# Kernel tuning notes

Hardware: AMD Instinct MI355X
Metric: run time of the kernel (lower is better)

Reference implementation:

```python
import jax, jax.numpy as jnp
import numpy as np

B, T, N, D = 4, 12, 512, 128
L = 4            # max_lag + 1 lag encoders
H = D // 2       # lag-encoder hidden dim
THRESHOLD = 0.1


def setup_inputs() -> dict:
    key = jax.random.key(0)
    ks = jax.random.split(key, 10)
    s = 0.02
    return {
        "x":   jax.random.normal(ks[0], (B, T, N, D), dtype=jnp.float32),
        # lag encoders: Linear(D->H), ReLU, Linear(H->D), stacked over L lags
        "W1":  s * jax.random.normal(ks[1], (L, D, H), dtype=jnp.float32),
        "b1":  jnp.zeros((L, H), dtype=jnp.float32),
        "W2":  s * jax.random.normal(ks[2], (L, H, D), dtype=jnp.float32),
        "b2":  jnp.zeros((L, D), dtype=jnp.float32),
        # causal scorer: Linear(2D->D), ReLU, (Dropout=id in eval), Linear(D->1), Sigmoid
        "Ws1": s * jax.random.normal(ks[3], (2 * D, D), dtype=jnp.float32),
        "bs1": jnp.zeros((D,), dtype=jnp.float32),
        "Ws2": s * jax.random.normal(ks[4], (D, 1), dtype=jnp.float32),
        "bs2": jnp.zeros((1,), dtype=jnp.float32),
    }


def reference(x, W1, b1, W2, b2, Ws1, bs1, Ws2, bs2):
    Tdim = x.shape[1]
    # lagged slices x[:, T-1-lag] for lag in 0..L-1 (all lags active since T > max_lag)
    lags = jnp.stack([x[:, max(0, Tdim - 1 - l)] for l in range(L)], axis=1)  # (B,L,N,D)
    h = jax.nn.relu(jnp.einsum('blnd,ldh->blnh', lags, W1) + b1[None, :, None, :])
    enc = jnp.einsum('blnh,lhd->blnd', h, W2) + b2[None, :, None, :]          # (B,L,N,D)
    agg = enc.mean(axis=1)                                                    # (B,N,D)

    # pairwise causal scorer. cat([src, tgt]) @ Ws1 == src @ Ws1[:D] + tgt @ Ws1[D:],
    # avoiding the explicit (B,N,N,2D) concat.
    src_proj = jnp.einsum('bnd,dk->bnk', agg, Ws1[:D])   # (B,N,D)
    tgt_proj = jnp.einsum('bnd,dk->bnk', agg, Ws1[D:])   # (B,N,D)
    pre = src_proj[:, :, None, :] + tgt_proj[:, None, :, :] + bs1  # (B,N,N,D)
    score = jax.nn.sigmoid(jnp.einsum('bijd,d->bij', jax.nn.relu(pre), Ws2[:, 0]) + bs2[0])

    # threshold sparsification + remove self loops
    adj = jnp.where(score > THRESHOLD, score, 0.0)
    adj = adj * (1.0 - jnp.eye(N, dtype=adj.dtype))

    # multi-hop propagation and global max normalization per batch element
    a2 = jnp.matmul(adj, adj)
    a3 = jnp.matmul(a2, adj)
    enhanced = adj + 0.5 * a2 + 0.25 * a3
    mx = jnp.max(enhanced, axis=(-1, -2), keepdims=True)
    return enhanced / (mx + 1e-8)
```

## Files before the change

### kernel.cpp

```cpp
#include <hip/hip_runtime.h>
#include <math.h>

#define Bn 4
#define Tn 12
#define Nn 512
#define Dn 128
#define Ln 4
#define Hn 64

typedef __attribute__((ext_vector_type(8))) short short8;
typedef __attribute__((ext_vector_type(4))) float f32x4;
typedef _Float16 h2 __attribute__((ext_vector_type(2)));

__device__ __forceinline__ unsigned short f2bf(float f) {
    unsigned int u = __float_as_uint(f);
    unsigned int r = (u + 0x7FFF + ((u >> 16) & 1)) >> 16;
    return (unsigned short)r;
}
__device__ __forceinline__ float bf2f(unsigned short s) {
    return __uint_as_float(((unsigned int)s) << 16);
}
__device__ __forceinline__ float fdot2(h2 a, h2 b, float c) {
#if defined(__has_builtin)
#if __has_builtin(__builtin_amdgcn_fdot2)
    return __builtin_amdgcn_fdot2(a, b, c, false);
#else
    return c + (float)a.x*(float)b.x + (float)a.y*(float)b.y;
#endif
#else
    return c + (float)a.x*(float)b.x + (float)a.y*(float)b.y;
#endif
}

__global__ __launch_bounds__(256) void k_prep(
    const float* __restrict__ W1, const float* __restrict__ W2, const float* __restrict__ Ws1,
    unsigned short* __restrict__ w1p, unsigned short* __restrict__ w2p,
    unsigned short* __restrict__ wsp)
{
    int g = blockIdx.x*256 + threadIdx.x;
    unsigned short tmp[8];
    if (g < 4096) {
        int lag = g >> 10, r = g & 1023;
        int n = r >> 4, k8 = r & 15;
        #pragma unroll
        for (int j = 0; j < 8; ++j) tmp[j] = f2bf(W1[(size_t)(lag*128 + k8*8 + j)*64 + n]);
        *(short8*)(w1p + (size_t)lag*8192 + n*128 + k8*8) = *(const short8*)tmp;
    } else if (g < 8192) {
        int r = g - 4096;
        int n = r >> 5, k8 = r & 31;
        #pragma unroll
        for (int j = 0; j < 8; ++j) tmp[j] = f2bf(W2[(size_t)(k8*8 + j)*128 + n]);
        *(short8*)(w2p + (size_t)n*256 + k8*8) = *(const short8*)tmp;
    } else {
        int r = g - 8192;
        int tgt = r >> 11, r2 = r & 2047;
        int n = r2 >> 4, k8 = r2 & 15;
        #pragma unroll
        for (int j = 0; j < 8; ++j) tmp[j] = f2bf(Ws1[(size_t)(tgt*128 + k8*8 + j)*128 + n]);
        *(short8*)(wsp + (size_t)tgt*16384 + n*128 + k8*8) = *(const short8*)tmp;
    }
}

__global__ __launch_bounds__(512) void k_enc(
    const float* __restrict__ x,  const float* __restrict__ b1,
    const float* __restrict__ b2, const float* __restrict__ bs1,
    const unsigned short* __restrict__ w1p, const unsigned short* __restrict__ w2p,
    const unsigned short* __restrict__ wsp,
    unsigned short* __restrict__ spb, unsigned short* __restrict__ tpb,
    unsigned int* __restrict__ maxslot)
{
    __shared__ __align__(16) unsigned short xAll[4][16*136];
    __shared__ __align__(16) unsigned short hA[16*264];
    __shared__ __align__(16) unsigned short aggA[16*136];
    int tid  = threadIdx.x;
    int bid  = blockIdx.x;
    int wv   = __builtin_amdgcn_readfirstlane(tid >> 6);
    int lane = tid & 63;
    if (bid == 0 && tid < Bn) maxslot[tid] = 0u;

    int r0 = bid * 16;
    int bb = r0 >> 9, n0 = r0 & 511;
    int m = lane & 15, q = lane >> 4;
    int colL = lane & 15, rq = lane >> 4;

    for (int v = tid; v < 2048; v += 512) {
        int lag = v >> 9, r = v & 511;
        int row = r >> 5, c4 = r & 31;
        const float4* xs = (const float4*)(x + ((size_t)(bb*Tn + (Tn-1-lag))*Nn + n0)*Dn);
        float4 f = xs[row*32 + c4];
        ushort4 o = { f2bf(f.x), f2bf(f.y), f2bf(f.z), f2bf(f.w) };
        *(ushort4*)&xAll[lag][row*136 + c4*4] = o;
    }
    __syncthreads();

    {
        int lag = wv >> 1, hf = wv & 1;
        f32x4 acc[2] = {{0.f,0.f,0.f,0.f},{0.f,0.f,0.f,0.f}};
        #pragma unroll
        for (int ks = 0; ks < 4; ++ks) {
            short8 af = *(const short8*)&xAll[lag][m*136 + ks*32 + q*8];
            #pragma unroll
            for (int nt = 0; nt < 2; ++nt) {
                short8 bg = *(const short8*)(w1p + (size_t)lag*8192 + (hf*32 + nt*16 + m)*128 + ks*32 + q*8);
                acc[nt] = __builtin_amdgcn_mfma_f32_16x16x32_bf16(af, bg, acc[nt], 0, 0, 0);
            }
        }
        #pragma unroll
        for (int nt = 0; nt < 2; ++nt) {
            int ncol = hf*32 + nt*16 + colL;
            float bv = b1[lag*Hn + ncol];
            #pragma unroll
            for (int reg = 0; reg < 4; ++reg)
                hA[(rq*4+reg)*264 + lag*64 + ncol] = f2bf(fmaxf(acc[nt][reg] + bv, 0.f));
        }
    }
    __syncthreads();

    {
        f32x4 acc = {0.f,0.f,0.f,0.f};
        #pragma unroll
        for (int ks = 0; ks < 8; ++ks) {
            short8 af = *(const short8*)&hA[m*264 + ks*32 + q*8];
            short8 bg = *(const short8*)(w2p + (size_t)(wv*16 + m)*256 + ks*32 + q*8);
            acc = __builtin_amdgcn_mfma_f32_16x16x32_bf16(af, bg, acc, 0, 0, 0);
        }
        int col = wv*16 + colL;
        float b2s = b2[col] + b2[Dn+col] + b2[2*Dn+col] + b2[3*Dn+col];
        #pragma unroll
        for (int reg = 0; reg < 4; ++reg)
            aggA[(rq*4+reg)*136 + col] = f2bf(0.25f*(acc[reg] + b2s));
    }
    __syncthreads();

    {
        int tgt = wv >> 2, wv4 = wv & 3;
        f32x4 acc[2] = {{0.f,0.f,0.f,0.f},{0.f,0.f,0.f,0.f}};
        #pragma unroll
        for (int ks = 0; ks < 4; ++ks) {
            short8 af = *(const short8*)&aggA[m*136 + ks*32 + q*8];
            #pragma unroll
            for (int nt = 0; nt < 2; ++nt) {
                short8 bg = *(const short8*)(wsp + (size_t)tgt*16384 + (wv4*32 + nt*16 + m)*128 + ks*32 + q*8);
                acc[nt] = __builtin_amdgcn_mfma_f32_16x16x32_bf16(af, bg, acc[nt], 0, 0, 0);
            }
        }
        unsigned short* dst = tgt ? tpb : spb;
        #pragma unroll
        for (int nt = 0; nt < 2; ++nt) {
            int n = wv4*32 + nt*16 + colL;
            float bv = tgt ? 0.f : bs1[n];
            #pragma unroll
            for (int reg = 0; reg < 4; ++reg) {
                _Float16 hv = (_Float16)(acc[nt][reg] + bv);
                dst[(size_t)(r0 + rq*4 + reg)*Dn + n] = __builtin_bit_cast(unsigned short, hv);
            }
        }
    }
}

__global__ __launch_bounds__(512) void k_score(
    const unsigned short* __restrict__ spb, const unsigned short* __restrict__ tpb,
    const float* __restrict__ Ws2, const float* __restrict__ bs2,
    unsigned short* __restrict__ adj_b, unsigned short* __restrict__ adj_pk)
{
    __shared__ unsigned int spl[64*65];
    __shared__ unsigned int tpl[64*65];
    __shared__ unsigned int wl[64];
    int tid = threadIdx.x;
    int wv = __builtin_amdgcn_readfirstlane(tid >> 6);
    int lane = tid & 63;
    int bz = blockIdx.z;
    int i0b = blockIdx.y * 64, j0b = blockIdx.x * 64;
    const unsigned short* spr = spb + (size_t)bz*Nn*Dn;
    const unsigned short* tpr = tpb + (size_t)bz*Nn*Dn;

    for (int v = tid; v < 1024; v += 512) {
        int row = v >> 4, c = v & 15;
        uint4 gs = *(const uint4*)(spr + (size_t)(i0b+row)*Dn + c*8);
        uint4 gt = *(const uint4*)(tpr + (size_t)(j0b+row)*Dn + c*8);
        spl[row*65 + c*4 + 0] = gs.x; spl[row*65 + c*4 + 1] = gs.y;
        spl[row*65 + c*4 + 2] = gs.z; spl[row*65 + c*4 + 3] = gs.w;
        tpl[row*65 + c*4 + 0] = gt.x; tpl[row*65 + c*4 + 1] = gt.y;
        tpl[row*65 + c*4 + 2] = gt.z; tpl[row*65 + c*4 + 3] = gt.w;
    }
    if (tid < 64) {
        h2 hw = { (_Float16)Ws2[tid*2], (_Float16)Ws2[tid*2+1] };
        wl[tid] = __builtin_bit_cast(unsigned int, hw);
    }
    __syncthreads();

    int iq = lane >> 4, jq = lane & 15;
    int iw = wv*8 + iq*2;
    float acc[2][4] = {};
    #pragma unroll 4
    for (int c = 0; c < 64; ++c) {
        h2 wp = __builtin_bit_cast(h2, wl[c]);
        h2 sh[2], th[4];
        #pragma unroll
        for (int ii = 0; ii < 2; ++ii) sh[ii] = __builtin_bit_cast(h2, spl[(iw+ii)*65 + c]);
        #pragma unroll
        for (int jj = 0; jj < 4; ++jj) th[jj] = __builtin_bit_cast(h2, tpl[(jq*4+jj)*65 + c]);
        #pragma unroll
        for (int ii = 0; ii < 2; ++ii)
            #pragma unroll
            for (int jj = 0; jj < 4; ++jj) {
                h2 r = __builtin_elementwise_max(sh[ii] + th[jj], (h2){(_Float16)0.f,(_Float16)0.f});
                acc[ii][jj] = fdot2(r, wp, acc[ii][jj]);
            }
    }
    float bsv = bs2[0];
    int i0 = i0b + iw;
    int j0 = j0b + jq*4;
    float vals[2][4];
    #pragma unroll
    for (int ii = 0; ii < 2; ++ii) {
        int i = i0 + ii;
        #pragma unroll
        for (int jj = 0; jj < 4; ++jj) {
            float z = acc[ii][jj] + bsv;
            float sc = 1.f/(1.f + __expf(-z));
            int j = j0 + jj;
            vals[ii][jj] = (sc > 0.1f && i != j) ? sc : 0.f;
        }
    }
    size_t base = (size_t)bz << 18;
    #pragma unroll
    for (int ii = 0; ii < 2; ++ii) {
        ushort4 rv = make_ushort4(f2bf(vals[ii][0]), f2bf(vals[ii][1]),
                                  f2bf(vals[ii][2]), f2bf(vals[ii][3]));
        *(ushort4*)(adj_b + base + (size_t)(i0+ii)*Nn + j0) = rv;
    }
    int kblk = i0 >> 5, qq = (i0 >> 3) & 3, t0 = i0 & 7;
    #pragma unroll
    for (int jj = 0; jj < 4; ++jj) {
        int j = j0 + jj;
        int jt = j >> 4, mm = j & 15;
        ushort2 cv = make_ushort2(f2bf(vals[0][jj]), f2bf(vals[1][jj]));
        *(ushort2*)(adj_pk + base + (size_t)(kblk*32 + jt)*512 + (qq*16 + mm)*8 + t0) = cv;
    }
}

__global__ __launch_bounds__(256) void k_mm1(
    const unsigned short* __restrict__ adj_b, const unsigned short* __restrict__ adj_pk,
    unsigned short* __restrict__ a2b)
{
    __shared__ unsigned short Als[2][64*72];
    int tid = threadIdx.x;
    int wv = __builtin_amdgcn_readfirstlane(tid >> 6);
    int lane = tid & 63;
    int b = blockIdx.z, i0 = blockIdx.y*64, j0 = blockIdx.x*64;
    size_t base = (size_t)b << 18;
    const unsigned short* Ab = adj_b + base;
    const unsigned short* pkB = adj_pk + base + (size_t)lane*8;
    int wm = wv >> 1, wn = wv & 1;
    int m = lane & 15, q = lane >> 4;
    int sr = tid >> 2, sc = (tid & 3)*16;
    int jtb = (j0 >> 4) + wn*2;
    f32x4 acc[2][2];
    #pragma unroll
    for (int mt = 0; mt < 2; ++mt)
        #pragma unroll
        for (int nt = 0; nt < 2; ++nt) acc[mt][nt] = (f32x4){0.f,0.f,0.f,0.f};

    *(short8*)&Als[0][sr*72 + sc]     = *(const short8*)(Ab + (size_t)(i0+sr)*Nn + sc);
    *(short8*)&Als[0][sr*72 + sc + 8] = *(const short8*)(Ab + (size_t)(i0+sr)*Nn + sc + 8);
    short8 pa0 = *(const short8*)(Ab + (size_t)(i0+sr)*Nn + 64 + sc);
    short8 pa1 = *(const short8*)(Ab + (size_t)(i0+sr)*Nn + 64 + sc + 8);
    short8 bfr[2][2][2];
    #pragma unroll
    for (int p = 0; p < 2; ++p)
        #pragma unroll
        for (int ks = 0; ks < 2; ++ks)
            #pragma unroll
            for (int nt = 0; nt < 2; ++nt)
                bfr[p][ks][nt] = *(const short8*)(pkB + (size_t)((p*2+ks)*32 + jtb + nt)*512);

    #pragma unroll
    for (int kt = 0; kt < 8; ++kt) {
        __syncthreads();
        if (kt < 7) {
            *(short8*)&Als[(kt+1)&1][sr*72 + sc]     = pa0;
            *(short8*)&Als[(kt+1)&1][sr*72 + sc + 8] = pa1;
        }
        if (kt < 6) {
            pa0 = *(const short8*)(Ab + (size_t)(i0+sr)*Nn + (kt+2)*64 + sc);
            pa1 = *(const short8*)(Ab + (size_t)(i0+sr)*Nn + (kt+2)*64 + sc + 8);
        }
        short8 cur[2][2];
        #pragma unroll
        for (int ks = 0; ks < 2; ++ks)
            #pragma unroll
            for (int nt = 0; nt < 2; ++nt) cur[ks][nt] = bfr[kt&1][ks][nt];
        if (kt < 6) {
            #pragma unroll
            for (int ks = 0; ks < 2; ++ks)
                #pragma unroll
                for (int nt = 0; nt < 2; ++nt)
                    bfr[kt&1][ks][nt] = *(const short8*)(pkB + (size_t)(((kt+2)*2+ks)*32 + jtb + nt)*512);
        }
        #pragma unroll
        for (int ks = 0; ks < 2; ++ks) {
            short8 af[2];
            #pragma unroll
            for (int mt = 0; mt < 2; ++mt)
                af[mt] = *(const short8*)&Als[kt&1][(wm*32+mt*16+m)*72 + ks*32 + q*8];
            #pragma unroll
            for (int mt = 0; mt < 2; ++mt)
                #pragma unroll
                for (int nt = 0; nt < 2; ++nt)
                    acc[mt][nt] = __builtin_amdgcn_mfma_f32_16x16x32_bf16(af[mt], cur[ks][nt], acc[mt][nt], 0, 0, 0);
        }
    }
    int col = lane & 15, rq = lane >> 4;
    #pragma unroll
    for (int mt = 0; mt < 2; ++mt)
        #pragma unroll
        for (int nt = 0; nt < 2; ++nt)
            #pragma unroll
            for (int reg = 0; reg < 4; ++reg) {
                int i = i0 + wm*32 + mt*16 + rq*4 + reg;
                int j = j0 + wn*32 + nt*16 + col;
                a2b[base + (size_t)i*Nn + j] = f2bf(acc[mt][nt][reg]);
            }
}

__global__ __launch_bounds__(256) void k_mm2(
    const unsigned short* __restrict__ adj_b, const unsigned short* __restrict__ adj_pk,
    const unsigned short* __restrict__ a2b,
    float* __restrict__ out, unsigned int* __restrict__ maxslot)
{
    __shared__ unsigned short Als[2][64*72];
    __shared__ float red[4];
    int tid = threadIdx.x;
    int wv = __builtin_amdgcn_readfirstlane(tid >> 6);
    int lane = tid & 63;
    int b = blockIdx.z, i0 = blockIdx.y*64, j0 = blockIdx.x*64;
    size_t base = (size_t)b << 18;
    const unsigned short* Ab = a2b + base;
    const unsigned short* pkB = adj_pk + base + (size_t)lane*8;
    int wm = wv >> 1, wn = wv & 1;
    int m = lane & 15, q = lane >> 4;
    int sr = tid >> 2, sc = (tid & 3)*16;
    int jtb = (j0 >> 4) + wn*2;
    f32x4 acc[2][2];
    #pragma unroll
    for (int mt = 0; mt < 2; ++mt)
        #pragma unroll
        for (int nt = 0; nt < 2; ++nt) acc[mt][nt] = (f32x4){0.f,0.f,0.f,0.f};

    *(short8*)&Als[0][sr*72 + sc]     = *(const short8*)(Ab + (size_t)(i0+sr)*Nn + sc);
    *(short8*)&Als[0][sr*72 + sc + 8] = *(const short8*)(Ab + (size_t)(i0+sr)*Nn + sc + 8);
    short8 pa0 = *(const short8*)(Ab + (size_t)(i0+sr)*Nn + 64 + sc);
    short8 pa1 = *(const short8*)(Ab + (size_t)(i0+sr)*Nn + 64 + sc + 8);
    short8 bfr[2][2][2];
    #pragma unroll
    for (int p = 0; p < 2; ++p)
        #pragma unroll
        for (int ks = 0; ks < 2; ++ks)
            #pragma unroll
            for (int nt = 0; nt < 2; ++nt)
                bfr[p][ks][nt] = *(const short8*)(pkB + (size_t)((p*2+ks)*32 + jtb + nt)*512);

    #pragma unroll
    for (int kt = 0; kt < 8; ++kt) {
        __syncthreads();
        if (kt < 7) {
            *(short8*)&Als[(kt+1)&1][sr*72 + sc]     = pa0;
            *(short8*)&Als[(kt+1)&1][sr*72 + sc + 8] = pa1;
        }
        if (kt < 6) {
            pa0 = *(const short8*)(Ab + (size_t)(i0+sr)*Nn + (kt+2)*64 + sc);
            pa1 = *(const short8*)(Ab + (size_t)(i0+sr)*Nn + (kt+2)*64 + sc + 8);
        }
        short8 cur[2][2];
        #pragma unroll
        for (int ks = 0; ks < 2; ++ks)
            #pragma unroll
            for (int nt = 0; nt < 2; ++nt) cur[ks][nt] = bfr[kt&1][ks][nt];
        if (kt < 6) {
            #pragma unroll
            for (int ks = 0; ks < 2; ++ks)
                #pragma unroll
                for (int nt = 0; nt < 2; ++nt)
                    bfr[kt&1][ks][nt] = *(const short8*)(pkB + (size_t)(((kt+2)*2+ks)*32 + jtb + nt)*512);
        }
        #pragma unroll
        for (int ks = 0; ks < 2; ++ks) {
            short8 af[2];
            #pragma unroll
            for (int mt = 0; mt < 2; ++mt)
                af[mt] = *(const short8*)&Als[kt&1][(wm*32+mt*16+m)*72 + ks*32 + q*8];
            #pragma unroll
            for (int mt = 0; mt < 2; ++mt)
                #pragma unroll
                for (int nt = 0; nt < 2; ++nt)
                    acc[mt][nt] = __builtin_amdgcn_mfma_f32_16x16x32_bf16(af[mt], cur[ks][nt], acc[mt][nt], 0, 0, 0);
        }
    }
    int col = lane & 15, rq = lane >> 4;
    float lmax = 0.f;
    const unsigned short* adjp = adj_b + base;
    #pragma unroll
    for (int mt = 0; mt < 2; ++mt)
        #pragma unroll
        for (int nt = 0; nt < 2; ++nt)
            #pragma unroll
            for (int reg = 0; reg < 4; ++reg) {
                int i = i0 + wm*32 + mt*16 + rq*4 + reg;
                int j = j0 + wn*32 + nt*16 + col;
                size_t off = (size_t)i*Nn + j;
                float e = bf2f(adjp[off]) + 0.5f*bf2f(Ab[off]) + 0.25f*acc[mt][nt][reg];
                out[base + off] = e;
                lmax = fmaxf(lmax, e);
            }
    #pragma unroll
    for (int s = 1; s < 64; s <<= 1) lmax = fmaxf(lmax, __shfl_xor(lmax, s, 64));
    if (lane == 0) red[wv] = lmax;
    __syncthreads();
    if (tid == 0) {
        float mx = fmaxf(fmaxf(red[0], red[1]), fmaxf(red[2], red[3]));
        atomicMax(maxslot + b, __float_as_uint(mx));
    }
}

__global__ __launch_bounds__(256) void k_norm(float* __restrict__ out,
                                              const unsigned int* __restrict__ maxslot)
{
    int idx = blockIdx.x*256 + threadIdx.x;
    int b = idx >> 16;
    float m = __uint_as_float(maxslot[b]);
    float inv = 1.f/(m + 1e-8f);
    float4* p = (float4*)out + idx;
    float4 v = *p;
    v.x *= inv; v.y *= inv; v.z *= inv; v.w *= inv;
    *p = v;
}

extern "C" void kernel_launch(void* const* d_in, const int* in_sizes, int n_in,
                              void* d_out, int out_size, void* d_ws, size_t ws_size,
                              hipStream_t stream) {
    const float* x   = (const float*)d_in[0];
    const float* W1  = (const float*)d_in[1];
    const float* b1  = (const float*)d_in[2];
    const float* W2  = (const float*)d_in[3];
    const float* b2  = (const float*)d_in[4];
    const float* Ws1 = (const float*)d_in[5];
    const float* bs1 = (const float*)d_in[6];
    const float* Ws2 = (const float*)d_in[7];
    const float* bs2 = (const float*)d_in[8];
    float* out = (float*)d_out;

    unsigned char* wsb = (unsigned char*)d_ws;
    unsigned short* spb    = (unsigned short*)(wsb);
    unsigned short* tpb    = (unsigned short*)(wsb + (512u<<10));
    unsigned short* adj_b  = (unsigned short*)(wsb + (1024u<<10));
    unsigned short* adj_pk = (unsigned short*)(wsb + (3072u<<10));
    unsigned short* a2b    = (unsigned short*)(wsb + (5120u<<10));
    unsigned int*   maxslot= (unsigned int*)(wsb + (7168u<<10));
    unsigned short* w1p    = (unsigned short*)(wsb + (7172u<<10));
    unsigned short* w2p    = (unsigned short*)(wsb + (7236u<<10));
    unsigned short* wsp    = (unsigned short*)(wsb + (7300u<<10));

    k_prep <<<dim3(48),       256, 0, stream>>>(W1, W2, Ws1, w1p, w2p, wsp);
    k_enc  <<<dim3(128),      512, 0, stream>>>(x, b1, b2, bs1, w1p, w2p, wsp, spb, tpb, maxslot);
    k_score<<<dim3(8, 8, Bn), 512, 0, stream>>>(spb, tpb, Ws2, bs2, adj_b, adj_pk);
    k_mm1  <<<dim3(8, 8, Bn), 256, 0, stream>>>(adj_b, adj_pk, a2b);
    k_mm2  <<<dim3(8, 8, Bn), 256, 0, stream>>>(adj_b, adj_pk, a2b, out, maxslot);
    k_norm <<<dim3(1024),     256, 0, stream>>>(out, maxslot);
}
```

Before: 111.9 us.

## Fuse max-normalization into k_mm2 via per-batch grid barrier

Removes the separate k_norm launch. Each k_mm2 block keeps its enhanced values in registers, publishes its local max, then spins on a per-batch counter until all 64 blocks of that batch have arrived, and writes the normalized output directly. This avoids writing the 4 MB fp32 output and reading it back, plus one kernel launch. The cost is a spin barrier that assumes all 256 blocks are co-resident, and blocks stall until the slowest tile of their batch finishes.

```diff
diff --git a/kernel.cpp b/kernel.cpp
--- a/kernel.cpp
+++ b/kernel.cpp
@@ -67,7 +67,7 @@
     const unsigned short* __restrict__ w1p, const unsigned short* __restrict__ w2p,
     const unsigned short* __restrict__ wsp,
     unsigned short* __restrict__ spb, unsigned short* __restrict__ tpb,
-    unsigned int* __restrict__ maxslot)
+    unsigned int* __restrict__ slots)
 {
     __shared__ __align__(16) unsigned short xAll[4][16*136];
     __shared__ __align__(16) unsigned short hA[16*264];
@@ -76,7 +76,7 @@
     int bid  = blockIdx.x;
     int wv   = __builtin_amdgcn_readfirstlane(tid >> 6);
     int lane = tid & 63;
-    if (bid == 0 && tid < Bn) maxslot[tid] = 0u;
+    if (bid == 0 && tid < 2*Bn) slots[tid] = 0u;
 
     int r0 = bid * 16;
     int bb = r0 >> 9, n0 = r0 & 511;
@@ -327,10 +327,11 @@
 __global__ __launch_bounds__(256) void k_mm2(
     const unsigned short* __restrict__ adj_b, const unsigned short* __restrict__ adj_pk,
     const unsigned short* __restrict__ a2b,
-    float* __restrict__ out, unsigned int* __restrict__ maxslot)
+    float* __restrict__ out, unsigned int* __restrict__ maxslot, unsigned int* __restrict__ done)
 {
     __shared__ unsigned short Als[2][64*72];
     __shared__ float red[4];
+    __shared__ float invs;
     int tid = threadIdx.x;
     int wv = __builtin_amdgcn_readfirstlane(tid >> 6);
     int lane = tid & 63;
@@ -410,7 +411,7 @@
                 int j = j0 + wn*32 + nt*16 + col;
                 size_t off = (size_t)i*Nn + j;
                 float e = bf2f(adjp[off]) + 0.5f*bf2f(Ab[off]) + 0.25f*acc[mt][nt][reg];
-                out[base + off] = e;
+                acc[mt][nt][reg] = e;
                 lmax = fmaxf(lmax, e);
             }
     #pragma unroll
@@ -420,20 +421,24 @@
     if (tid == 0) {
         float mx = fmaxf(fmaxf(red[0], red[1]), fmaxf(red[2], red[3]));
         atomicMax(maxslot + b, __float_as_uint(mx));
-    }
-}
-
-__global__ __launch_bounds__(256) void k_norm(float* __restrict__ out,
-                                              const unsigned int* __restrict__ maxslot)
-{
-    int idx = blockIdx.x*256 + threadIdx.x;
-    int b = idx >> 16;
-    float m = __uint_as_float(maxslot[b]);
-    float inv = 1.f/(m + 1e-8f);
-    float4* p = (float4*)out + idx;
-    float4 v = *p;
-    v.x *= inv; v.y *= inv; v.z *= inv; v.w *= inv;
-    *p = v;
+        __hip_atomic_fetch_add(done + b, 1u, __ATOMIC_ACQ_REL, __HIP_MEMORY_SCOPE_AGENT);
+        while (__hip_atomic_load(done + b, __ATOMIC_ACQUIRE, __HIP_MEMORY_SCOPE_AGENT) < 64u)
+            __builtin_amdgcn_s_sleep(1);
+        unsigned int mu = __hip_atomic_load(maxslot + b, __ATOMIC_ACQUIRE, __HIP_MEMORY_SCOPE_AGENT);
+        invs = 1.f / (__uint_as_float(mu) + 1e-8f);
+    }
+    __syncthreads();
+    float inv = invs;
+    #pragma unroll
+    for (int mt = 0; mt < 2; ++mt)
+        #pragma unroll
+        for (int nt = 0; nt < 2; ++nt)
+            #pragma unroll
+            for (int reg = 0; reg < 4; ++reg) {
+                int i = i0 + wm*32 + mt*16 + rq*4 + reg;
+                int j = j0 + wn*32 + nt*16 + col;
+                out[base + (size_t)i*Nn + j] = acc[mt][nt][reg] * inv;
+            }
 }
 
 extern "C" void kernel_launch(void* const* d_in, const int* in_sizes, int n_in,
@@ -456,15 +461,16 @@
     unsigned short* adj_b  = (unsigned short*)(wsb + (1024u<<10));
     unsigned short* adj_pk = (unsigned short*)(wsb + (3072u<<10));
     unsigned short* a2b    = (unsigned short*)(wsb + (5120u<<10));
-    unsigned int*   maxslot= (unsigned int*)(wsb + (7168u<<10));
+    unsigned int*   slots  = (unsigned int*)(wsb + (7168u<<10));
     unsigned short* w1p    = (unsigned short*)(wsb + (7172u<<10));
     unsigned short* w2p    = (unsigned short*)(wsb + (7236u<<10));
     unsigned short* wsp    = (unsigned short*)(wsb + (7300u<<10));
+    unsigned int*   maxslot = slots;
+    unsigned int*   done    = slots + 4;
 
     k_prep <<<dim3(48),       256, 0, stream>>>(W1, W2, Ws1, w1p, w2p, wsp);
-    k_enc  <<<dim3(128),      512, 0, stream>>>(x, b1, b2, bs1, w1p, w2p, wsp, spb, tpb, maxslot);
+    k_enc  <<<dim3(128),      512, 0, stream>>>(x, b1, b2, bs1, w1p, w2p, wsp, spb, tpb, slots);
     k_score<<<dim3(8, 8, Bn), 512, 0, stream>>>(spb, tpb, Ws2, bs2, adj_b, adj_pk);
     k_mm1  <<<dim3(8, 8, Bn), 256, 0, stream>>>(adj_b, adj_pk, a2b);
-    k_mm2  <<<dim3(8, 8, Bn), 256, 0, stream>>>(adj_b, adj_pk, a2b, out, maxslot);
-    k_norm <<<dim3(1024),     256, 0, stream>>>(out, maxslot);
-}
+    k_mm2  <<<dim3(8, 8, Bn), 256, 0, stream>>>(adj_b, adj_pk, a2b, out, maxslot, done);
+}
```

Measured after the change: 120.0 us. +7.2%, slower.
